# Kernel optimization log

Hardware: AMD Instinct MI355X
Metric: run time of the kernel (lower is better)

## Reference

```python
import jax, jax.numpy as jnp
import numpy as np

N_NODES = 100000
N_EDGES = 6400000
D_FEAT = 128
OUT_DIM = 128


def setup_inputs() -> dict:
    key = jax.random.key(0)
    k1, k2, k3, k4, k5, k6 = jax.random.split(key, 6)
    V_node = jax.random.normal(k1, (N_NODES, D_FEAT), dtype=jnp.float32)
    senders = jax.random.randint(k2, (N_EDGES,), 0, N_NODES, dtype=jnp.int32)
    receivers = jax.random.randint(k3, (N_EDGES,), 0, N_NODES, dtype=jnp.int32)
    edge_features = jax.random.normal(k4, (N_EDGES, 2), dtype=jnp.float32)
    # Dense params: input dim = D_FEAT + 2 (concat of V_node and net_current)
    fan_in = D_FEAT + 2
    W = jax.random.normal(k5, (fan_in, OUT_DIM), dtype=jnp.float32) / np.sqrt(fan_in)
    b = jnp.zeros((OUT_DIM,), dtype=jnp.float32)
    return {"V_node": V_node, "senders": senders, "receivers": receivers,
            "edge_features": edge_features, "W": W, "b": b}


def reference(V_node, senders, receivers, edge_features, W, b):
    num_nodes = V_node.shape[0]
    # KVL: edge voltage = V[recv] - V[send], complex as [re, im]
    V2 = V_node[..., :2]
    V_edge = V2[receivers] - V2[senders]          # [E, 2]
    # Ohm's law: I = Y * V (complex multiply)
    G, B_ = edge_features[..., 0], edge_features[..., 1]
    V_re, V_im = V_edge[..., 0], V_edge[..., 1]
    I_edge = jnp.stack([G * V_re - B_ * V_im,
                        G * V_im + B_ * V_re], axis=-1)  # [E, 2]
    # KCL: net current into each node
    I_in = jax.ops.segment_sum(I_edge, receivers, num_segments=num_nodes)
    I_out = jax.ops.segment_sum(I_edge, senders, num_segments=num_nodes)
    net_current = I_in - I_out                    # [N, 2]
    node_inputs = jnp.concatenate([V_node, net_current], axis=-1)  # [N, D+2]
    V_node_out = jax.nn.relu(node_inputs @ W + b)  # [N, OUT_DIM]
    return (V_node_out, I_edge, V_edge)
```

## Files before the change

kernel.cpp:

```cpp
#include <hip/hip_runtime.h>

#define NNODES 100000
#define NEDGES 6400000
#define NPAIRS (NEDGES / 2)
#define NQUAD  (NEDGES / 8)
#define DFEAT 128
#define ODIM 128

#define FXSCALE 2048.0f
#define INV_FXSCALE (1.0f / 2048.0f)
#define FBIAS 65536
#define FMASK 0x3FFFFFFULL

#define RANGE 16384
#define NRANGE 7
#define NC_MAX 36

typedef unsigned long long ull;

__device__ __forceinline__ int qfx(float x) {
    return min(max(__float2int_rn(x * FXSCALE), -FBIAS), FBIAS - 1);
}

__global__ __launch_bounds__(256) void prep_kernel(const float* __restrict__ Vn,
                                                   float2* __restrict__ v2) {
    int i = blockIdx.x * 256 + threadIdx.x;
    if (i < NNODES)
        v2[i] = make_float2(Vn[i * DFEAT + 0], Vn[i * DFEAT + 1]);
}

__global__ __launch_bounds__(256) void stream_kernel(const int4* __restrict__ s4,
                                                     const int4* __restrict__ r4,
                                                     const float4* __restrict__ ef2,
                                                     const float2* __restrict__ v2,
                                                     float4* __restrict__ I2,
                                                     float4* __restrict__ V2e) {
    int t = blockIdx.x * 256 + threadIdx.x;
    if (t >= NQUAD) return;
    int4 sA = s4[2 * t], sB = s4[2 * t + 1];
    int4 rA = r4[2 * t], rB = r4[2 * t + 1];
    int p = 4 * t;
    float4 e0 = ef2[p + 0], e1 = ef2[p + 1], e2 = ef2[p + 2], e3 = ef2[p + 3];

    float2 vr0 = v2[rA.x], vr1 = v2[rA.y], vr2 = v2[rA.z], vr3 = v2[rA.w];
    float2 vr4 = v2[rB.x], vr5 = v2[rB.y], vr6 = v2[rB.z], vr7 = v2[rB.w];
    float2 vs0 = v2[sA.x], vs1 = v2[sA.y], vs2 = v2[sA.z], vs3 = v2[sA.w];
    float2 vs4 = v2[sB.x], vs5 = v2[sB.y], vs6 = v2[sB.z], vs7 = v2[sB.w];

#define EDGE(vex, vey, ire, iim, vr, vs, G, B)       \
    float vex = vr.x - vs.x, vey = vr.y - vs.y;      \
    float ire = G * vex - B * vey;                   \
    float iim = G * vey + B * vex;

    EDGE(x0, y0, a0, b0, vr0, vs0, e0.x, e0.y)
    EDGE(x1, y1, a1, b1, vr1, vs1, e0.z, e0.w)
    EDGE(x2, y2, a2, b2, vr2, vs2, e1.x, e1.y)
    EDGE(x3, y3, a3, b3, vr3, vs3, e1.z, e1.w)
    EDGE(x4, y4, a4, b4, vr4, vs4, e2.x, e2.y)
    EDGE(x5, y5, a5, b5, vr5, vs5, e2.z, e2.w)
    EDGE(x6, y6, a6, b6, vr6, vs6, e3.x, e3.y)
    EDGE(x7, y7, a7, b7, vr7, vs7, e3.z, e3.w)
#undef EDGE

    V2e[p + 0] = make_float4(x0, y0, x1, y1);
    V2e[p + 1] = make_float4(x2, y2, x3, y3);
    V2e[p + 2] = make_float4(x4, y4, x5, y5);
    V2e[p + 3] = make_float4(x6, y6, x7, y7);
    I2[p + 0]  = make_float4(a0, b0, a1, b1);
    I2[p + 1]  = make_float4(a2, b2, a3, b3);
    I2[p + 2]  = make_float4(a4, b4, a5, b5);
    I2[p + 3]  = make_float4(a6, b6, a7, b7);
}

__global__ __launch_bounds__(1024) void reduce_kernel(const int2* __restrict__ s2,
                                                      const int2* __restrict__ r2,
                                                      const float4* __restrict__ I2,
                                                      ull* __restrict__ partial,
                                                      int NC, int ppc) {
    __shared__ ull acc[RANGE];
    const int ri   = blockIdx.y;
    const int base = ri * RANGE;
    for (int i = threadIdx.x; i < RANGE; i += 1024) acc[i] = 0ULL;
    __syncthreads();

    const int p0 = blockIdx.x * ppc;
    const int p1 = min(p0 + ppc, NPAIRS);
    for (int p = p0 + threadIdx.x; p < p1; p += 1024) {
        int2 ss = s2[p];
        int2 rr = r2[p];
        float4 II = I2[p];

        int re0 = qfx(II.x), im0 = qfx(II.y);
        int re1 = qfx(II.z), im1 = qfx(II.w);

        int d;
        d = rr.x - base;
        if ((unsigned)d < RANGE)
            atomicAdd(&acc[d], (1ULL << 52)
                | ((ull)(unsigned)(FBIAS + re0) << 26) | (unsigned)(FBIAS + im0));
        d = ss.x - base;
        if ((unsigned)d < RANGE)
            atomicAdd(&acc[d], (1ULL << 52)
                | ((ull)(unsigned)(FBIAS - re0) << 26) | (unsigned)(FBIAS - im0));
        d = rr.y - base;
        if ((unsigned)d < RANGE)
            atomicAdd(&acc[d], (1ULL << 52)
                | ((ull)(unsigned)(FBIAS + re1) << 26) | (unsigned)(FBIAS + im1));
        d = ss.y - base;
        if ((unsigned)d < RANGE)
            atomicAdd(&acc[d], (1ULL << 52)
                | ((ull)(unsigned)(FBIAS - re1) << 26) | (unsigned)(FBIAS - im1));
    }
    __syncthreads();

    ull* dst = partial + ((size_t)(ri * NC + blockIdx.x)) * RANGE;
    for (int i = threadIdx.x; i < RANGE; i += 1024) dst[i] = acc[i];
}

__global__ __launch_bounds__(256) void decode_kernel(const ull* __restrict__ partial,
                                                     float2* __restrict__ net,
                                                     int NC) {
    int n = blockIdx.x * 256 + threadIdx.x;
    if (n >= NNODES) return;
    int ri = n >> 14;
    int idx = n & (RANGE - 1);
    ull p = 0ULL;
    for (int c = 0; c < NC; ++c)
        p += partial[((size_t)(ri * NC + c)) * RANGE + idx];
    int cnt   = (int)(p >> 52);
    int re_fx = (int)((p >> 26) & FMASK) - (cnt << 16);
    int im_fx = (int)(p & FMASK) - (cnt << 16);
    net[n] = make_float2((float)re_fx * INV_FXSCALE, (float)im_fx * INV_FXSCALE);
}

#define BN 64
#define TPAD 132

__global__ __launch_bounds__(256) void mlp_kernel(const float* __restrict__ Vn,
                                                  const float2* __restrict__ net,
                                                  const float* __restrict__ W,
                                                  const float* __restrict__ b,
                                                  float* __restrict__ out) {
    __shared__ float tile[BN][TPAD];
    const int n0 = blockIdx.x * BN;
    const int tid = threadIdx.x;

    for (int i = tid; i < BN * (DFEAT / 4); i += 256) {
        int node = i >> 5;
        int k4 = (i & 31) * 4;
        int gn = n0 + node;
        float4 v;
        if (gn < NNODES) v = *reinterpret_cast<const float4*>(&Vn[gn * DFEAT + k4]);
        else             v = make_float4(0.f, 0.f, 0.f, 0.f);
        *reinterpret_cast<float4*>(&tile[node][k4]) = v;
    }
    if (tid < BN) {
        int gn = n0 + tid;
        float2 nc = (gn < NNODES) ? net[gn] : make_float2(0.f, 0.f);
        tile[tid][128] = nc.x;
        tile[tid][129] = nc.y;
    }
    __syncthreads();

    const int lane = tid & 63;
    const int col0 = __builtin_amdgcn_readfirstlane((tid >> 6) * 32);

    float acc[32];
#pragma unroll
    for (int c = 0; c < 32; ++c) acc[c] = b[col0 + c];

    for (int k = 0; k < DFEAT; k += 4) {
        float4 in4 = *reinterpret_cast<const float4*>(&tile[lane][k]);
#pragma unroll
        for (int c = 0; c < 32; ++c) {
            acc[c] += in4.x * W[(k + 0) * ODIM + col0 + c];
            acc[c] += in4.y * W[(k + 1) * ODIM + col0 + c];
            acc[c] += in4.z * W[(k + 2) * ODIM + col0 + c];
            acc[c] += in4.w * W[(k + 3) * ODIM + col0 + c];
        }
    }
    {
        float nx = tile[lane][128];
        float ny = tile[lane][129];
#pragma unroll
        for (int c = 0; c < 32; ++c) {
            acc[c] += nx * W[128 * ODIM + col0 + c];
            acc[c] += ny * W[129 * ODIM + col0 + c];
        }
    }

    __syncthreads();
#pragma unroll
    for (int c = 0; c < 32; ++c) tile[lane][col0 + c] = fmaxf(acc[c], 0.f);
    __syncthreads();

    for (int i = tid; i < BN * (ODIM / 4); i += 256) {
        int node = i >> 5;
        int k4 = (i & 31) * 4;
        int gn = n0 + node;
        if (gn < NNODES)
            *reinterpret_cast<float4*>(&out[gn * ODIM + k4]) =
                *reinterpret_cast<const float4*>(&tile[node][k4]);
    }
}

extern "C" void kernel_launch(void* const* d_in, const int* in_sizes, int n_in,
                              void* d_out, int out_size, void* d_ws, size_t ws_size,
                              hipStream_t stream) {
    const float* V_node      = (const float*)d_in[0];
    const int*   senders     = (const int*)d_in[1];
    const int*   receivers   = (const int*)d_in[2];
    const float* edge_feats  = (const float*)d_in[3];
    const float* W           = (const float*)d_in[4];
    const float* b           = (const float*)d_in[5];

    float*  out_V  = (float*)d_out;
    float*  out_I  = out_V + (size_t)NNODES * ODIM;
    float*  out_Ve = out_I + (size_t)NEDGES * 2;

    float2* net = (float2*)d_ws;
    float2* v2  = net + NNODES;
    ull* partial = (ull*)(v2 + NNODES);

    size_t reserved  = 2 * (size_t)NNODES * sizeof(float2);
    size_t per_chunk = (size_t)NRANGE * RANGE * sizeof(ull);
    int NC = (ws_size > reserved) ? (int)((ws_size - reserved) / per_chunk) : 1;
    if (NC > NC_MAX) NC = NC_MAX;
    if (NC < 1) NC = 1;
    int ppc = (NPAIRS + NC - 1) / NC;

    prep_kernel<<<(NNODES + 255) / 256, 256, 0, stream>>>(V_node, v2);
    stream_kernel<<<(NQUAD + 255) / 256, 256, 0, stream>>>(
        (const int4*)senders, (const int4*)receivers, (const float4*)edge_feats,
        v2, (float4*)out_I, (float4*)out_Ve);
    dim3 gridB(NC, NRANGE);
    reduce_kernel<<<gridB, 1024, 0, stream>>>(
        (const int2*)senders, (const int2*)receivers, (const float4*)out_I,
        partial, NC, ppc);
    decode_kernel<<<(NNODES + 255) / 256, 256, 0, stream>>>(partial, net, NC);
    mlp_kernel<<<(NNODES + BN - 1) / BN, 256, 0, stream>>>(V_node, net, W, b, out_V);
}
```

Before: 231.9 us.

## Use bf16 MFMA for node MLP and fuse partial-sum decode into it

Replaces the scalar fp32 FMA dense layer with bf16 MFMA 16x16x32 instructions, using a bf16-transposed W prepared in the prep kernel. The decode of per-chunk atomic partials is folded into the MLP kernel, removing a separate launch and the net buffer. The node range partition is retuned to fewer, larger ranges with more chunks. Rounding activations and weights to bf16 reduces accuracy, and the per-column output stores are less coalesced than before.

Result: faster. 226.0 us (-2.6%).

```diff
diff --git a/kernel.cpp b/kernel.cpp
--- a/kernel.cpp
+++ b/kernel.cpp
@@ -12,21 +12,33 @@
 #define FBIAS 65536
 #define FMASK 0x3FFFFFFULL
 
-#define RANGE 16384
-#define NRANGE 7
-#define NC_MAX 36
+#define RANGE 18688
+#define NRANGE 6
+#define NC_MAX 42
 
 typedef unsigned long long ull;
+typedef __attribute__((ext_vector_type(8))) short short8;
+typedef __attribute__((ext_vector_type(4))) float f32x4;
 
 __device__ __forceinline__ int qfx(float x) {
     return min(max(__float2int_rn(x * FXSCALE), -FBIAS), FBIAS - 1);
 }
+__device__ __forceinline__ unsigned short f2b(float f) {
+    unsigned u = __float_as_uint(f);
+    return (unsigned short)((u + 0x7FFFu + ((u >> 16) & 1u)) >> 16);
+}
 
 __global__ __launch_bounds__(256) void prep_kernel(const float* __restrict__ Vn,
-                                                   float2* __restrict__ v2) {
+                                                   const float* __restrict__ W,
+                                                   float2* __restrict__ v2,
+                                                   unsigned short* __restrict__ wt) {
     int i = blockIdx.x * 256 + threadIdx.x;
     if (i < NNODES)
         v2[i] = make_float2(Vn[i * DFEAT + 0], Vn[i * DFEAT + 1]);
+    if (i < 128 * 128) {
+        int col = i >> 7, k = i & 127;
+        wt[col * 128 + k] = f2b(W[k * ODIM + col]);
+    }
 }
 
 __global__ __launch_bounds__(256) void stream_kernel(const int4* __restrict__ s4,
@@ -117,90 +129,91 @@
     for (int i = threadIdx.x; i < RANGE; i += 1024) dst[i] = acc[i];
 }
 
-__global__ __launch_bounds__(256) void decode_kernel(const ull* __restrict__ partial,
-                                                     float2* __restrict__ net,
-                                                     int NC) {
-    int n = blockIdx.x * 256 + threadIdx.x;
-    if (n >= NNODES) return;
-    int ri = n >> 14;
-    int idx = n & (RANGE - 1);
-    ull p = 0ULL;
-    for (int c = 0; c < NC; ++c)
-        p += partial[((size_t)(ri * NC + c)) * RANGE + idx];
-    int cnt   = (int)(p >> 52);
-    int re_fx = (int)((p >> 26) & FMASK) - (cnt << 16);
-    int im_fx = (int)(p & FMASK) - (cnt << 16);
-    net[n] = make_float2((float)re_fx * INV_FXSCALE, (float)im_fx * INV_FXSCALE);
-}
-
-#define BN 64
-#define TPAD 132
+#define TPADW 136
 
 __global__ __launch_bounds__(256) void mlp_kernel(const float* __restrict__ Vn,
-                                                  const float2* __restrict__ net,
+                                                  const ull* __restrict__ partial,
+                                                  const unsigned short* __restrict__ wt,
                                                   const float* __restrict__ W,
-                                                  const float* __restrict__ b,
-                                                  float* __restrict__ out) {
-    __shared__ float tile[BN][TPAD];
-    const int n0 = blockIdx.x * BN;
+                                                  const float* __restrict__ bg,
+                                                  float* __restrict__ out,
+                                                  int NC) {
+    __shared__ unsigned short A_lds[64 * TPADW];
+    __shared__ unsigned short Wt_lds[128 * TPADW];
+    __shared__ float2 net_lds[64];
+
     const int tid = threadIdx.x;
-
-    for (int i = tid; i < BN * (DFEAT / 4); i += 256) {
-        int node = i >> 5;
-        int k4 = (i & 31) * 4;
+    const int n0 = blockIdx.x * 64;
+
+    for (int i = tid; i < 64 * 32; i += 256) {
+        int node = i >> 5, k4 = (i & 31) * 4;
         int gn = n0 + node;
-        float4 v;
-        if (gn < NNODES) v = *reinterpret_cast<const float4*>(&Vn[gn * DFEAT + k4]);
-        else             v = make_float4(0.f, 0.f, 0.f, 0.f);
-        *reinterpret_cast<float4*>(&tile[node][k4]) = v;
-    }
-    if (tid < BN) {
-        int gn = n0 + tid;
-        float2 nc = (gn < NNODES) ? net[gn] : make_float2(0.f, 0.f);
-        tile[tid][128] = nc.x;
-        tile[tid][129] = nc.y;
+        float4 v = (gn < NNODES)
+            ? *reinterpret_cast<const float4*>(&Vn[(size_t)gn * DFEAT + k4])
+            : make_float4(0.f, 0.f, 0.f, 0.f);
+        ushort4 h = {f2b(v.x), f2b(v.y), f2b(v.z), f2b(v.w)};
+        *reinterpret_cast<ushort4*>(&A_lds[node * TPADW + k4]) = h;
+    }
+    for (int i = tid; i < 128 * 16; i += 256) {
+        int col = i >> 4, ch = i & 15;
+        *reinterpret_cast<short8*>(&Wt_lds[col * TPADW + ch * 8]) =
+            *reinterpret_cast<const short8*>(&wt[col * 128 + ch * 8]);
+    }
+    if (tid < 64) {
+        int n = n0 + tid;
+        float2 nc = make_float2(0.f, 0.f);
+        if (n < NNODES) {
+            int ri = n / RANGE, idx = n - ri * RANGE;
+            ull p = 0ULL;
+            for (int c = 0; c < NC; ++c)
+                p += partial[((size_t)(ri * NC + c)) * RANGE + idx];
+            int cnt   = (int)(p >> 52);
+            int re_fx = (int)((p >> 26) & FMASK) - (cnt << 16);
+            int im_fx = (int)(p & FMASK) - (cnt << 16);
+            nc = make_float2((float)re_fx * INV_FXSCALE,
+                             (float)im_fx * INV_FXSCALE);
+        }
+        net_lds[tid] = nc;
     }
     __syncthreads();
 
     const int lane = tid & 63;
-    const int col0 = __builtin_amdgcn_readfirstlane((tid >> 6) * 32);
-
-    float acc[32];
-#pragma unroll
-    for (int c = 0; c < 32; ++c) acc[c] = b[col0 + c];
-
-    for (int k = 0; k < DFEAT; k += 4) {
-        float4 in4 = *reinterpret_cast<const float4*>(&tile[lane][k]);
-#pragma unroll
-        for (int c = 0; c < 32; ++c) {
-            acc[c] += in4.x * W[(k + 0) * ODIM + col0 + c];
-            acc[c] += in4.y * W[(k + 1) * ODIM + col0 + c];
-            acc[c] += in4.z * W[(k + 2) * ODIM + col0 + c];
-            acc[c] += in4.w * W[(k + 3) * ODIM + col0 + c];
+    const int w    = tid >> 6;
+    const int q    = lane >> 4;
+    const int c15  = lane & 15;
+
+    short8 afr[4];
+#pragma unroll
+    for (int kk = 0; kk < 4; ++kk)
+        afr[kk] = *reinterpret_cast<const short8*>(
+            &A_lds[(w * 16 + c15) * TPADW + kk * 32 + q * 8]);
+
+    float2 nets[4];
+#pragma unroll
+    for (int r = 0; r < 4; ++r)
+        nets[r] = net_lds[w * 16 + q * 4 + r];
+
+#pragma unroll
+    for (int ct = 0; ct < 8; ++ct) {
+        int col = ct * 16 + c15;
+        float bc = bg[col];
+        f32x4 acc = {bc, bc, bc, bc};
+#pragma unroll
+        for (int kk = 0; kk < 4; ++kk) {
+            short8 bfr = *reinterpret_cast<const short8*>(
+                &Wt_lds[col * TPADW + kk * 32 + q * 8]);
+            acc = __builtin_amdgcn_mfma_f32_16x16x32_bf16(afr[kk], bfr, acc, 0, 0, 0);
         }
-    }
-    {
-        float nx = tile[lane][128];
-        float ny = tile[lane][129];
-#pragma unroll
-        for (int c = 0; c < 32; ++c) {
-            acc[c] += nx * W[128 * ODIM + col0 + c];
-            acc[c] += ny * W[129 * ODIM + col0 + c];
+        float w128c = W[128 * ODIM + col];
+        float w129c = W[129 * ODIM + col];
+#pragma unroll
+        for (int r = 0; r < 4; ++r) {
+            int node = n0 + w * 16 + q * 4 + r;
+            float v = acc[r] + nets[r].x * w128c + nets[r].y * w129c;
+            v = fmaxf(v, 0.f);
+            if (node < NNODES)
+                out[(size_t)node * ODIM + col] = v;
         }
-    }
-
-    __syncthreads();
-#pragma unroll
-    for (int c = 0; c < 32; ++c) tile[lane][col0 + c] = fmaxf(acc[c], 0.f);
-    __syncthreads();
-
-    for (int i = tid; i < BN * (ODIM / 4); i += 256) {
-        int node = i >> 5;
-        int k4 = (i & 31) * 4;
-        int gn = n0 + node;
-        if (gn < NNODES)
-            *reinterpret_cast<float4*>(&out[gn * ODIM + k4]) =
-                *reinterpret_cast<const float4*>(&tile[node][k4]);
     }
 }
 
@@ -218,18 +231,18 @@
     float*  out_I  = out_V + (size_t)NNODES * ODIM;
     float*  out_Ve = out_I + (size_t)NEDGES * 2;
 
-    float2* net = (float2*)d_ws;
-    float2* v2  = net + NNODES;
-    ull* partial = (ull*)(v2 + NNODES);
-
-    size_t reserved  = 2 * (size_t)NNODES * sizeof(float2);
+    float2* v2 = (float2*)d_ws;
+    unsigned short* wt = (unsigned short*)(v2 + NNODES);
+    ull* partial = (ull*)((char*)d_ws + 800000 + 32768);
+
+    size_t reserved  = 800000 + 32768;
     size_t per_chunk = (size_t)NRANGE * RANGE * sizeof(ull);
     int NC = (ws_size > reserved) ? (int)((ws_size - reserved) / per_chunk) : 1;
     if (NC > NC_MAX) NC = NC_MAX;
     if (NC < 1) NC = 1;
     int ppc = (NPAIRS + NC - 1) / NC;
 
-    prep_kernel<<<(NNODES + 255) / 256, 256, 0, stream>>>(V_node, v2);
+    prep_kernel<<<(NNODES + 255) / 256, 256, 0, stream>>>(V_node, W, v2, wt);
     stream_kernel<<<(NQUAD + 255) / 256, 256, 0, stream>>>(
         (const int4*)senders, (const int4*)receivers, (const float4*)edge_feats,
         v2, (float4*)out_I, (float4*)out_Ve);
@@ -237,6 +250,6 @@
     reduce_kernel<<<gridB, 1024, 0, stream>>>(
         (const int2*)senders, (const int2*)receivers, (const float4*)out_I,
         partial, NC, ppc);
-    decode_kernel<<<(NNODES + 255) / 256, 256, 0, stream>>>(partial, net, NC);
-    mlp_kernel<<<(NNODES + BN - 1) / BN, 256, 0, stream>>>(V_node, net, W, b, out_V);
-}
+    mlp_kernel<<<(NNODES + 63) / 64, 256, 0, stream>>>(
+        V_node, partial, wt, W, b, out_V, NC);
+}
```
